# Performance work log

Hardware: AMD Instinct MI355X
Metric: run time of the kernel (lower is better)

## Reference

```python
import jax, jax.numpy as jnp
import numpy as np
from jax import lax

NUM_GROUP = 2048
INIT_DIST = 1.0e10


def setup_inputs() -> dict:
    key = jax.random.key(0)
    k1, k2 = jax.random.split(key)
    B, N = 32, 100000
    xyz = jax.random.normal(k1, (B, N, 3), dtype=jnp.float32)
    farthest_init = jax.random.randint(k2, (B,), 0, N, dtype=jnp.int64)
    return {"xyz": xyz, "farthest_init": farthest_init}


def reference(xyz, farthest_init):
    # xyz: [B, N, 3], farthest_init: [B] initial farthest indices
    B, N, _ = xyz.shape
    farthest0 = farthest_init.astype(jnp.int32)
    dist0 = jnp.full((B, N), INIT_DIST, dtype=xyz.dtype)

    def step(carry, _):
        distance, farthest = carry
        # gather current centroid per batch: [B, 1, 3]
        centroid = jnp.take_along_axis(xyz, farthest[:, None, None], axis=1)
        d = jnp.sum((xyz - centroid) ** 2, axis=-1)          # [B, N]
        distance = jnp.minimum(distance, d)                   # masked update
        new_farthest = jnp.argmax(distance, axis=-1).astype(jnp.int32)
        return (distance, new_farthest), farthest

    (_, _), cent_t = lax.scan(step, (dist0, farthest0), None, length=NUM_GROUP)
    centroids = cent_t.T                                      # [B, num_group]
    sampled = jnp.take_along_axis(xyz, centroids[:, :, None], axis=1)  # [B, num_group, 3]
    return sampled
```

## Files before the change

kernel.cpp:

```cpp
#include <hip/hip_runtime.h>

#pragma clang fp contract(off)

#define BATCH 32
#define NPTS 100000
#define NGROUP 2048
#define NBLK_PER_BATCH 8
#define NPB (NPTS / NBLK_PER_BATCH)
#define TPB 512
#define NPT 25
#define TAIL (NPB - (NPT - 1) * TPB)
#define NQUAD 7
#define QTOT (NPB / 4)
#define QTAIL (QTOT - (NQUAD - 1) * TPB)

typedef unsigned long long u64;
typedef unsigned int u32;

static_assert(NPB * NBLK_PER_BATCH == NPTS, "block split must be exact");
static_assert(QTOT * 4 == NPB, "quad split must be exact");

__device__ __forceinline__ float fsub_x(float a, float b) {
  float r; asm("v_sub_f32 %0, %1, %2" : "=v"(r) : "v"(a), "v"(b)); return r;
}
__device__ __forceinline__ float fmul_x(float a, float b) {
  float r; asm("v_mul_f32 %0, %1, %2" : "=v"(r) : "v"(a), "v"(b)); return r;
}
__device__ __forceinline__ float fma_x(float a, float b, float c) {
  float r; asm("v_fma_f32 %0, %1, %2, %3" : "=v"(r) : "v"(a), "v"(b), "v"(c)); return r;
}

#define LD_AG(p)    __hip_atomic_load((p),  __ATOMIC_RELAXED, __HIP_MEMORY_SCOPE_AGENT)
#define ST_AG(p,v)  __hip_atomic_store((p), (v), __ATOMIC_RELAXED, __HIP_MEMORY_SCOPE_AGENT)

__global__ __launch_bounds__(TPB, 1)
void fps_kernel(const float* __restrict__ xyz,
                const int* __restrict__ finit,
                float* __restrict__ out,
                u64* __restrict__ slots)
{
  const int blk  = blockIdx.x;
  const int b    = blk & (BATCH - 1);
  const int j    = blk >> 5;
  const int tid  = threadIdx.x;
  const int lane = tid & 63;
  const int wid  = tid >> 6;

  __shared__ __align__(16) float sx[NPB];
  __shared__ __align__(16) float sy[NPB];
  __shared__ __align__(16) float sz[NPB];
  __shared__ u64   sval[8];
  __shared__ float scoord[3];

  const float* xb = xyz + (size_t)b * NPTS * 3;
  const int base = j * NPB;

#pragma unroll
  for (int i = 0; i < NPT; ++i) {
    const bool valid = (i < NPT - 1) || (tid < TAIL);
    const int p = tid + i * TPB;
    if (valid) {
      const int gp = base + p;
      sx[p] = xb[gp * 3 + 0];
      sy[p] = xb[gp * 3 + 1];
      sz[p] = xb[gp * 3 + 2];
    }
  }
  float pd[NQUAD * 4];
#pragma unroll
  for (int q = 0; q < NQUAD; ++q) {
    const bool vq = (q < NQUAD - 1) || (tid < QTAIL);
#pragma unroll
    for (int k = 0; k < 4; ++k) pd[q * 4 + k] = vq ? 1.0e10f : -1.0f;
  }
  __syncthreads();

  const int cur0 = finit[b];
  float cx = xb[cur0 * 3 + 0], cy = xb[cur0 * 3 + 1], cz = xb[cur0 * 3 + 2];

  u64* gs = slots + (size_t)b * 2 * NBLK_PER_BATCH;

  for (int t = 0; t < NGROUP; ++t) {
    if (j == 0 && wid == 1 && lane == 0) {
      float* o = out + ((size_t)b * NGROUP + t) * 3;
      o[0] = cx; o[1] = cy; o[2] = cz;
    }
    if (t == NGROUP - 1) break;

    const int p   = t & 1;
    const u32 tag = (u32)(t & 0x7FFF);

    float bestv = -1.0f;
    int   besti = 0x7fffffff;
#pragma unroll
    for (int q = 0; q < NQUAD; ++q) {
      int qi = tid + q * TPB;
      if (q == NQUAD - 1 && tid >= QTAIL) qi = 0;
      const int pb = qi * 4;
      const float4 vx = *(const float4*)&sx[pb];
      const float4 vy = *(const float4*)&sy[pb];
      const float4 vz = *(const float4*)&sz[pb];
#define POINT(K, XK, YK, ZK)                                                  \
      {                                                                       \
        const float dx = fsub_x(XK, cx);                                      \
        const float dy = fsub_x(YK, cy);                                      \
        const float dz = fsub_x(ZK, cz);                                      \
        const float d  = fma_x(dz, dz, fma_x(dy, dy, fmul_x(dx, dx)));        \
        const float nd = fminf(pd[q * 4 + K], d);                             \
        pd[q * 4 + K] = nd;                                                   \
        if (nd > bestv) { bestv = nd; besti = base + pb + K; }                \
      }
      POINT(0, vx.x, vy.x, vz.x)
      POINT(1, vx.y, vy.y, vz.y)
      POINT(2, vx.z, vy.z, vz.z)
      POINT(3, vx.w, vy.w, vz.w)
#undef POINT
    }

    u64 pk = ((u64)__float_as_uint(bestv) << 32) | (u64)((~(u32)besti) & 0x1FFFFu);
#pragma unroll
    for (int off = 32; off > 0; off >>= 1) {
      const u64 o = __shfl_xor(pk, off, 64);
      if (o > pk) pk = o;
    }
    if (lane == 0) sval[wid] = pk;
    __syncthreads();

    if (wid == 0) {
      u64 sv = (lane < 8) ? sval[lane] : 0ull;
#pragma unroll
      for (int off = 4; off > 0; off >>= 1) {
        const u64 o = __shfl_xor(sv, off, 64);
        if (o > sv) sv = o;
      }
      if (lane == 0) ST_AG(gs + p * NBLK_PER_BATCH + j, sv | ((u64)tag << 17));
      u64 gv;
      do {
        gv = (lane < NBLK_PER_BATCH) ? LD_AG(gs + p * NBLK_PER_BATCH + lane) : 0ull;
      } while (!__all(lane >= NBLK_PER_BATCH || (((u32)(gv >> 17) & 0x7FFFu) == tag)));

      float fx = 0.f, fy = 0.f, fz = 0.f;
      if (lane < NBLK_PER_BATCH) {
        const int cand = (int)((~(u32)gv) & 0x1FFFFu);
        const float* cp = xb + (size_t)cand * 3;
        fx = cp[0]; fy = cp[1]; fz = cp[2];
      }
      u64 win = gv;
#pragma unroll
      for (int off = 4; off > 0; off >>= 1) {
        const u64 o = __shfl_xor(win, off, 64);
        if (o > win) win = o;
      }
      const u64 wmax = __shfl(win, 0, 64);
      const u64 mask = __ballot(lane < NBLK_PER_BATCH && gv == wmax);
      const int w    = (int)__ffsll((long long)mask) - 1;
      const float ncx = __shfl(fx, w, 64);
      const float ncy = __shfl(fy, w, 64);
      const float ncz = __shfl(fz, w, 64);
      if (lane == 0) { scoord[0] = ncx; scoord[1] = ncy; scoord[2] = ncz; }
    }
    __syncthreads();

    cx = scoord[0]; cy = scoord[1]; cz = scoord[2];
  }
}

extern "C" void kernel_launch(void* const* d_in, const int* in_sizes, int n_in,
                              void* d_out, int out_size, void* d_ws, size_t ws_size,
                              hipStream_t stream) {
  const float* xyz   = (const float*)d_in[0];
  const int*   finit = (const int*)d_in[1];
  float*       out   = (float*)d_out;
  u64*         slots = (u64*)d_ws;

  hipMemsetAsync(d_ws, 0xFF,
                 (size_t)BATCH * 2 * NBLK_PER_BATCH * sizeof(u64), stream);

  fps_kernel<<<dim3(BATCH * NBLK_PER_BATCH), dim3(TPB), 0, stream>>>(xyz, finit, out, slots);
}
```

Measured before the change: 4.992 ms.

## Replace block barriers with per-wave global slots and LDS flag release

Each wave now publishes its argmax candidate straight to a global slot array (64 slots per batch) instead of reducing through shared memory behind a __syncthreads. Wave 0 of every block polls all 64 slots, picks the winner, and releases the new centroid to the other waves through tagged shared-memory words they spin on. This removes both per-iteration block barriers. In exchange there are more global atomic stores and wider polling, and non-zero waves spin on LDS.

```diff
diff --git a/kernel.cpp b/kernel.cpp
--- a/kernel.cpp
+++ b/kernel.cpp
@@ -13,6 +13,7 @@
 #define NQUAD 7
 #define QTOT (NPB / 4)
 #define QTAIL (QTOT - (NQUAD - 1) * TPB)
+#define NWAVE 64
 
 typedef unsigned long long u64;
 typedef unsigned int u32;
@@ -30,6 +31,8 @@
   float r; asm("v_fma_f32 %0, %1, %2, %3" : "=v"(r) : "v"(a), "v"(b), "v"(c)); return r;
 }
 
+#define LD_WG(p)    __hip_atomic_load((p),  __ATOMIC_RELAXED, __HIP_MEMORY_SCOPE_WORKGROUP)
+#define ST_WG(p,v)  __hip_atomic_store((p), (v), __ATOMIC_RELAXED, __HIP_MEMORY_SCOPE_WORKGROUP)
 #define LD_AG(p)    __hip_atomic_load((p),  __ATOMIC_RELAXED, __HIP_MEMORY_SCOPE_AGENT)
 #define ST_AG(p,v)  __hip_atomic_store((p), (v), __ATOMIC_RELAXED, __HIP_MEMORY_SCOPE_AGENT)
 
@@ -45,12 +48,14 @@
   const int tid  = threadIdx.x;
   const int lane = tid & 63;
   const int wid  = tid >> 6;
+  const int gw   = j * 8 + wid;
 
   __shared__ __align__(16) float sx[NPB];
   __shared__ __align__(16) float sy[NPB];
   __shared__ __align__(16) float sz[NPB];
-  __shared__ u64   sval[8];
-  __shared__ float scoord[3];
+  __shared__ u64 srel[2][3];
+
+  if (tid < 6) srel[tid / 3][tid % 3] = ~0ull;
 
   const float* xb = xyz + (size_t)b * NPTS * 3;
   const int base = j * NPB;
@@ -78,7 +83,7 @@
   const int cur0 = finit[b];
   float cx = xb[cur0 * 3 + 0], cy = xb[cur0 * 3 + 1], cz = xb[cur0 * 3 + 2];
 
-  u64* gs = slots + (size_t)b * 2 * NBLK_PER_BATCH;
+  u64* gs = slots + (size_t)b * 2 * NWAVE;
 
   for (int t = 0; t < NGROUP; ++t) {
     if (j == 0 && wid == 1 && lane == 0) {
@@ -123,45 +128,46 @@
       const u64 o = __shfl_xor(pk, off, 64);
       if (o > pk) pk = o;
     }
-    if (lane == 0) sval[wid] = pk;
-    __syncthreads();
+    if (lane == 0) ST_AG(gs + p * NWAVE + gw, pk | ((u64)tag << 17));
 
+    float ncx, ncy, ncz;
     if (wid == 0) {
-      u64 sv = (lane < 8) ? sval[lane] : 0ull;
-#pragma unroll
-      for (int off = 4; off > 0; off >>= 1) {
-        const u64 o = __shfl_xor(sv, off, 64);
-        if (o > sv) sv = o;
-      }
-      if (lane == 0) ST_AG(gs + p * NBLK_PER_BATCH + j, sv | ((u64)tag << 17));
       u64 gv;
       do {
-        gv = (lane < NBLK_PER_BATCH) ? LD_AG(gs + p * NBLK_PER_BATCH + lane) : 0ull;
-      } while (!__all(lane >= NBLK_PER_BATCH || (((u32)(gv >> 17) & 0x7FFFu) == tag)));
+        gv = LD_AG(gs + p * NWAVE + lane);
+      } while (!__all(((u32)(gv >> 17) & 0x7FFFu) == tag));
 
-      float fx = 0.f, fy = 0.f, fz = 0.f;
-      if (lane < NBLK_PER_BATCH) {
-        const int cand = (int)((~(u32)gv) & 0x1FFFFu);
-        const float* cp = xb + (size_t)cand * 3;
-        fx = cp[0]; fy = cp[1]; fz = cp[2];
-      }
+      const int cand = (int)((~(u32)gv) & 0x1FFFFu);
+      const float* cp = xb + (size_t)cand * 3;
+      const float fx = cp[0], fy = cp[1], fz = cp[2];
+
       u64 win = gv;
 #pragma unroll
-      for (int off = 4; off > 0; off >>= 1) {
+      for (int off = 32; off > 0; off >>= 1) {
         const u64 o = __shfl_xor(win, off, 64);
         if (o > win) win = o;
       }
       const u64 wmax = __shfl(win, 0, 64);
-      const u64 mask = __ballot(lane < NBLK_PER_BATCH && gv == wmax);
+      const u64 mask = __ballot(gv == wmax);
       const int w    = (int)__ffsll((long long)mask) - 1;
-      const float ncx = __shfl(fx, w, 64);
-      const float ncy = __shfl(fy, w, 64);
-      const float ncz = __shfl(fz, w, 64);
-      if (lane == 0) { scoord[0] = ncx; scoord[1] = ncy; scoord[2] = ncz; }
+      ncx = __shfl(fx, w, 64); ncy = __shfl(fy, w, 64); ncz = __shfl(fz, w, 64);
+
+      if (lane == 0) {
+        const u64 lo = (u64)tag << 17;
+        ST_WG(&srel[p][0], ((u64)__float_as_uint(ncx) << 32) | lo);
+        ST_WG(&srel[p][1], ((u64)__float_as_uint(ncy) << 32) | lo);
+        ST_WG(&srel[p][2], ((u64)__float_as_uint(ncz) << 32) | lo);
+      }
+    } else {
+      u64 rv;
+      do {
+        rv = (lane < 3) ? LD_WG(&srel[p][lane]) : 0ull;
+      } while (!__all(lane >= 3 || (((u32)(rv >> 17) & 0x7FFFu) == tag)));
+      const float f = __uint_as_float((u32)(rv >> 32));
+      ncx = __shfl(f, 0, 64); ncy = __shfl(f, 1, 64); ncz = __shfl(f, 2, 64);
     }
-    __syncthreads();
 
-    cx = scoord[0]; cy = scoord[1]; cz = scoord[2];
+    cx = ncx; cy = ncy; cz = ncz;
   }
 }
 
@@ -173,8 +179,7 @@
   float*       out   = (float*)d_out;
   u64*         slots = (u64*)d_ws;
 
-  hipMemsetAsync(d_ws, 0xFF,
-                 (size_t)BATCH * 2 * NBLK_PER_BATCH * sizeof(u64), stream);
+  hipMemsetAsync(d_ws, 0xFF, (size_t)BATCH * 2 * NWAVE * sizeof(u64), stream);
 
   fps_kernel<<<dim3(BATCH * NBLK_PER_BATCH), dim3(TPB), 0, stream>>>(xyz, finit, out, slots);
 }
```

Measured after the change: 7.082 ms. 1.42x slower.
